# Kernel tuning notes

Measured on AMD Instinct MI355X. Metric: run time of the kernel, lower is better.

The kernel has to match this reference:

```python
import jax, jax.numpy as jnp
import numpy as np

T, H, E, F = 2048, 2048, 8, 4096  # tokens, hidden, experts, ffn per expert


def setup_inputs() -> dict:
    key = jax.random.key(0)
    ks = jax.random.split(key, 5)
    scale = 0.02
    return {
        "x": jax.random.normal(ks[0], (T, H), dtype=jnp.float32),
        "gate_w": jax.random.normal(ks[1], (E, H), dtype=jnp.float32) * scale,
        "w1": jax.random.normal(ks[2], (E * F, H), dtype=jnp.float32) * scale,
        "w2": jax.random.normal(ks[3], (E * F, H), dtype=jnp.float32) * scale,
        "w3": jax.random.normal(ks[4], (E * F, H), dtype=jnp.float32) * scale,
        "top_k": 2,
    }


def reference(x, gate_w, w1, w2, w3, top_k):
    # x: [T, H]; gate_w: [E, H]; w1/w2/w3: [E*F, H]
    t, h = x.shape
    e = gate_w.shape[0]
    f = w1.shape[0] // e

    # --- routing (matches select_experts / dense_forward gating) ---
    gate_logits = x @ gate_w.T                                   # [T, E]
    probs = jax.nn.softmax(gate_logits.astype(jnp.float32), axis=-1)
    vals, idx = jax.lax.top_k(probs, top_k)                      # [T, k]
    vals = vals / vals.sum(axis=-1, keepdims=True)               # renormalize
    w_full = jnp.zeros((t, e), dtype=probs.dtype)
    w_full = w_full.at[jnp.arange(t)[:, None], idx].set(vals)    # [T, E]

    # --- expert FFN: SwiGLU per expert (full-capacity, no token drop) ---
    w1r = w1.reshape(e, f, h)
    w3r = w3.reshape(e, f, h)
    w2r = w2.reshape(e, f, h)
    h1 = jnp.einsum('th,efh->etf', x, w1r)                       # [E, T, F]
    h3 = jnp.einsum('th,efh->etf', x, w3r)
    inter = jax.nn.silu(h1) * h3                                 # [E, T, F]
    out_e = jnp.einsum('etf,efh->eth', inter, w2r)               # [E, T, H]

    # --- combine with routing weights ---
    out = jnp.einsum('eth,te->th', out_e, w_full.astype(x.dtype))
    return out
```

## Files before the change

kernel.cpp:

```cpp
#include <hip/hip_runtime.h>
#include <cstdint>
#include <cstddef>

#define T_TOK 2048
#define H_DIM 2048
#define E_NUM 8
#define F_DIM 4096

typedef __attribute__((ext_vector_type(8))) short bh8;
typedef __attribute__((ext_vector_type(4))) float f32x4;

static __device__ __forceinline__ unsigned short f2bf(float f) {
  union { float f; unsigned int u; } v; v.f = f;
  unsigned int r = v.u + 0x7FFFu + ((v.u >> 16) & 1u);
  return (unsigned short)(r >> 16);
}

__global__ __launch_bounds__(256) void convert_x(const float* __restrict__ x,
                                                 unsigned short* __restrict__ xb) {
  size_t i = ((size_t)blockIdx.x * 256 + threadIdx.x) * 4;
  float4 v = *(const float4*)(x + i);
  ushort4 o;
  o.x = f2bf(v.x); o.y = f2bf(v.y); o.z = f2bf(v.z); o.w = f2bf(v.w);
  *(ushort4*)(xb + i) = o;
}

__global__ __launch_bounds__(64) void gate_topk(const float* __restrict__ x,
                                                const float* __restrict__ gw,
                                                int* __restrict__ counts,
                                                int* __restrict__ etok,
                                                float* __restrict__ ewts) {
  const int t = blockIdx.x;
  const int lane = threadIdx.x;
  float acc[E_NUM];
#pragma unroll
  for (int e = 0; e < E_NUM; e++) acc[e] = 0.f;
  const float* xr = x + (size_t)t * H_DIM;
  for (int i = lane; i < H_DIM; i += 64) {
    float xv = xr[i];
#pragma unroll
    for (int e = 0; e < E_NUM; e++) acc[e] += xv * gw[e * H_DIM + i];
  }
#pragma unroll
  for (int e = 0; e < E_NUM; e++) {
#pragma unroll
    for (int off = 32; off > 0; off >>= 1) acc[e] += __shfl_xor(acc[e], off, 64);
  }
  if (lane == 0) {
    int e0 = 0;
#pragma unroll
    for (int e = 1; e < E_NUM; e++) if (acc[e] > acc[e0]) e0 = e;
    int e1 = (e0 == 0) ? 1 : 0;
#pragma unroll
    for (int e = 0; e < E_NUM; e++) {
      if (e != e0 && acc[e] > acc[e1]) e1 = e;
    }
    float z = __expf(acc[e1] - acc[e0]);
    float w0 = 1.f / (1.f + z);
    float w1v = z / (1.f + z);
    int p0 = atomicAdd(&counts[e0], 1);
    etok[e0 * T_TOK + p0] = t; ewts[e0 * T_TOK + p0] = w0;
    int p1 = atomicAdd(&counts[e1], 1);
    etok[e1 * T_TOK + p1] = t; ewts[e1 * T_TOK + p1] = w1v;
  }
}

__global__ void scan_offsets(const int* __restrict__ counts, int* __restrict__ offsets) {
  if (threadIdx.x == 0 && blockIdx.x == 0) {
    int run = 0;
    for (int e = 0; e < E_NUM; e++) { offsets[e] = run; run += counts[e]; }
  }
}

__global__ __launch_bounds__(256) void gemm1_swiglu(
    const unsigned short* __restrict__ xb,
    const float* __restrict__ w1,
    const float* __restrict__ w3,
    const int* __restrict__ counts, const int* __restrict__ offsets,
    const int* __restrict__ etok,
    unsigned short* __restrict__ inter)
{
  const int e = blockIdx.z, mt = blockIdx.y, nt = blockIdx.x;
  const int cnt = counts[e];
  const int rem = cnt - mt * 128;
  if (rem <= 0) return;
  const int tid = threadIdx.x;
  const int lane = tid & 63;
  const int wv = tid >> 6;

  __shared__ alignas(16) unsigned short As[128][40];
  __shared__ alignas(16) unsigned short B1s[64][40];
  __shared__ alignas(16) unsigned short B3s[64][40];

  const int ar0 = tid >> 2;
  const int ar1 = 64 + (tid >> 2);
  const int ac8 = (tid & 3) * 8;
  const int tokbase = e * T_TOK + mt * 128;
  const int t0 = etok[tokbase + (ar0 < rem ? ar0 : rem - 1)];
  const int t1 = etok[tokbase + (ar1 < rem ? ar1 : rem - 1)];
  const unsigned short* a0p = xb + (size_t)t0 * H_DIM + ac8;
  const unsigned short* a1p = xb + (size_t)t1 * H_DIM + ac8;

  const int br0 = tid >> 3;
  const int br1 = 32 + (tid >> 3);
  const int bc4 = (tid & 7) * 4;
  const size_t wrow0 = ((size_t)(e * F_DIM + nt * 64 + br0)) * H_DIM + bc4;
  const size_t wrow1 = ((size_t)(e * F_DIM + nt * 64 + br1)) * H_DIM + bc4;

  const int wm = (wv >> 1) * 64;
  const int wn = (wv & 1) * 32;
  const int mrow = lane & 15;
  const int qk = (lane >> 4) * 8;

  f32x4 acc1[4][2], acc3[4][2];
#pragma unroll
  for (int i = 0; i < 4; i++)
#pragma unroll
    for (int j = 0; j < 2; j++) { acc1[i][j] = (f32x4)(0.f); acc3[i][j] = (f32x4)(0.f); }

  for (int k0 = 0; k0 < H_DIM; k0 += 32) {
    *(uint4*)&As[ar0][ac8] = *(const uint4*)(a0p + k0);
    *(uint4*)&As[ar1][ac8] = *(const uint4*)(a1p + k0);
    {
      float4 v0 = *(const float4*)(w1 + wrow0 + k0);
      float4 v1 = *(const float4*)(w1 + wrow1 + k0);
      float4 u0 = *(const float4*)(w3 + wrow0 + k0);
      float4 u1 = *(const float4*)(w3 + wrow1 + k0);
      ushort4 o;
      o.x = f2bf(v0.x); o.y = f2bf(v0.y); o.z = f2bf(v0.z); o.w = f2bf(v0.w);
      *(ushort4*)&B1s[br0][bc4] = o;
      o.x = f2bf(v1.x); o.y = f2bf(v1.y); o.z = f2bf(v1.z); o.w = f2bf(v1.w);
      *(ushort4*)&B1s[br1][bc4] = o;
      o.x = f2bf(u0.x); o.y = f2bf(u0.y); o.z = f2bf(u0.z); o.w = f2bf(u0.w);
      *(ushort4*)&B3s[br0][bc4] = o;
      o.x = f2bf(u1.x); o.y = f2bf(u1.y); o.z = f2bf(u1.z); o.w = f2bf(u1.w);
      *(ushort4*)&B3s[br1][bc4] = o;
    }
    __syncthreads();
    bh8 a[4], b1[2], b3[2];
#pragma unroll
    for (int i = 0; i < 4; i++) a[i] = *(const bh8*)&As[wm + i * 16 + mrow][qk];
#pragma unroll
    for (int j = 0; j < 2; j++) {
      b1[j] = *(const bh8*)&B1s[wn + j * 16 + mrow][qk];
      b3[j] = *(const bh8*)&B3s[wn + j * 16 + mrow][qk];
    }
#pragma unroll
    for (int i = 0; i < 4; i++)
#pragma unroll
      for (int j = 0; j < 2; j++) {
        acc1[i][j] = __builtin_amdgcn_mfma_f32_16x16x32_bf16(a[i], b1[j], acc1[i][j], 0, 0, 0);
        acc3[i][j] = __builtin_amdgcn_mfma_f32_16x16x32_bf16(a[i], b3[j], acc3[i][j], 0, 0, 0);
      }
    __syncthreads();
  }

  const int off = offsets[e];
  const int quad = lane >> 4;
#pragma unroll
  for (int i = 0; i < 4; i++) {
#pragma unroll
    for (int r = 0; r < 4; r++) {
      int m = wm + i * 16 + quad * 4 + r;
      if (m < rem) {
        size_t rowbase = (size_t)(off + mt * 128 + m) * F_DIM + nt * 64 + wn + mrow;
#pragma unroll
        for (int j = 0; j < 2; j++) {
          float c1 = acc1[i][j][r], c3 = acc3[i][j][r];
          float s = c1 / (1.f + __expf(-c1));
          inter[rowbase + j * 16] = f2bf(s * c3);
        }
      }
    }
  }
}

__global__ __launch_bounds__(256) void gemm2_scatter(
    const unsigned short* __restrict__ inter,
    const float* __restrict__ w2,
    const int* __restrict__ counts, const int* __restrict__ offsets,
    const int* __restrict__ etok, const float* __restrict__ ewts,
    float* __restrict__ out)
{
  const int e = blockIdx.z, mt = blockIdx.y, nt = blockIdx.x;
  const int cnt = counts[e];
  const int rem = cnt - mt * 128;
  if (rem <= 0) return;
  const int tid = threadIdx.x;
  const int lane = tid & 63;
  const int wv = tid >> 6;

  __shared__ alignas(16) unsigned short As[128][40];
  __shared__ alignas(16) unsigned short Bs[128][40];

  const int off = offsets[e];
  const int ar0 = tid >> 2;
  const int ar1 = 64 + (tid >> 2);
  const int ac8 = (tid & 3) * 8;
  const int g0 = off + mt * 128 + (ar0 < rem ? ar0 : rem - 1);
  const int g1 = off + mt * 128 + (ar1 < rem ? ar1 : rem - 1);
  const unsigned short* a0p = inter + (size_t)g0 * F_DIM + ac8;
  const unsigned short* a1p = inter + (size_t)g1 * F_DIM + ac8;

  const int bkr = tid >> 5;
  const int bc4 = (tid & 31) * 4;

  const int wm = (wv >> 1) * 64;
  const int wn = (wv & 1) * 64;
  const int mrow = lane & 15;
  const int qk = (lane >> 4) * 8;

  f32x4 acc[4][4];
#pragma unroll
  for (int i = 0; i < 4; i++)
#pragma unroll
    for (int j = 0; j < 4; j++) acc[i][j] = (f32x4)(0.f);

  for (int k0 = 0; k0 < F_DIM; k0 += 32) {
    *(uint4*)&As[ar0][ac8] = *(const uint4*)(a0p + k0);
    *(uint4*)&As[ar1][ac8] = *(const uint4*)(a1p + k0);
#pragma unroll
    for (int l = 0; l < 4; l++) {
      int krow = bkr + l * 8;
      float4 v = *(const float4*)(w2 + ((size_t)(e * F_DIM + k0 + krow)) * H_DIM + nt * 128 + bc4);
      Bs[bc4 + 0][krow] = f2bf(v.x);
      Bs[bc4 + 1][krow] = f2bf(v.y);
      Bs[bc4 + 2][krow] = f2bf(v.z);
      Bs[bc4 + 3][krow] = f2bf(v.w);
    }
    __syncthreads();
    bh8 a[4], b[4];
#pragma unroll
    for (int i = 0; i < 4; i++) a[i] = *(const bh8*)&As[wm + i * 16 + mrow][qk];
#pragma unroll
    for (int j = 0; j < 4; j++) b[j] = *(const bh8*)&Bs[wn + j * 16 + mrow][qk];
#pragma unroll
    for (int i = 0; i < 4; i++)
#pragma unroll
      for (int j = 0; j < 4; j++)
        acc[i][j] = __builtin_amdgcn_mfma_f32_16x16x32_bf16(a[i], b[j], acc[i][j], 0, 0, 0);
    __syncthreads();
  }

  const int quad = lane >> 4;
#pragma unroll
  for (int i = 0; i < 4; i++) {
#pragma unroll
    for (int r = 0; r < 4; r++) {
      int m = wm + i * 16 + quad * 4 + r;
      if (m < rem) {
        int slot = e * T_TOK + mt * 128 + m;
        int t = etok[slot];
        float wgt = ewts[slot];
        float* orow = out + (size_t)t * H_DIM + nt * 128 + wn + mrow;
#pragma unroll
        for (int j = 0; j < 4; j++) atomicAdd(orow + j * 16, wgt * acc[i][j][r]);
      }
    }
  }
}

extern "C" void kernel_launch(void* const* d_in, const int* in_sizes, int n_in,
                              void* d_out, int out_size, void* d_ws, size_t ws_size,
                              hipStream_t stream) {
  const float* x  = (const float*)d_in[0];
  const float* gw = (const float*)d_in[1];
  const float* w1 = (const float*)d_in[2];
  const float* w2 = (const float*)d_in[3];
  const float* w3 = (const float*)d_in[4];
  float* out = (float*)d_out;

  char* ws = (char*)d_ws;
  int* counts   = (int*)(ws + 0);
  int* offsets  = (int*)(ws + 64);
  int* etok     = (int*)(ws + 128);
  float* ewts   = (float*)(ws + 128 + 65536);
  unsigned short* xb    = (unsigned short*)(ws + 256 * 1024);
  unsigned short* inter = (unsigned short*)(ws + 256 * 1024 + 8 * 1024 * 1024);

  hipMemsetAsync(counts, 0, 64, stream);
  hipMemsetAsync(d_out, 0, (size_t)T_TOK * H_DIM * sizeof(float), stream);

  convert_x<<<(T_TOK * H_DIM) / (256 * 4), 256, 0, stream>>>(x, xb);
  gate_topk<<<T_TOK, 64, 0, stream>>>(x, gw, counts, etok, ewts);
  scan_offsets<<<1, 64, 0, stream>>>(counts, offsets);
  gemm1_swiglu<<<dim3(F_DIM / 64, 16, E_NUM), 256, 0, stream>>>(xb, w1, w3, counts, offsets, etok, inter);
  gemm2_scatter<<<dim3(H_DIM / 128, 16, E_NUM), 256, 0, stream>>>(inter, w2, counts, offsets, etok, ewts, out);
}
```

Before: 1.386 ms.

## Pre-convert expert weights to bf16 and pre-transpose w2 in workspace

Adds pre-pass kernels that convert w1 and w3 to bf16 and transpose plus convert w2 into a K-contiguous bf16 layout, when the workspace is large enough. The GEMM kernels then load bf16 tiles with 16-byte vector loads instead of converting fp32 per tile. Every expert weight tile is reread by up to 16 M-tile blocks, so converting once is meant to cut fp32 traffic and the strided scalar LDS writes in gemm2. The pre-pass still reads all 768MB of fp32 weights every call and writes bf16 copies, so it adds traffic of its own. The output atomics also switch to unsafeAtomicAdd for hardware float atomics.

```diff
diff --git a/kernel.cpp b/kernel.cpp
--- a/kernel.cpp
+++ b/kernel.cpp
@@ -16,13 +16,41 @@
   return (unsigned short)(r >> 16);
 }
 
-__global__ __launch_bounds__(256) void convert_x(const float* __restrict__ x,
-                                                 unsigned short* __restrict__ xb) {
+__global__ __launch_bounds__(256) void convert_f32_bf16(const float* __restrict__ src,
+                                                        unsigned short* __restrict__ dst) {
   size_t i = ((size_t)blockIdx.x * 256 + threadIdx.x) * 4;
-  float4 v = *(const float4*)(x + i);
+  float4 v = *(const float4*)(src + i);
   ushort4 o;
   o.x = f2bf(v.x); o.y = f2bf(v.y); o.z = f2bf(v.z); o.w = f2bf(v.w);
-  *(ushort4*)(xb + i) = o;
+  *(ushort4*)(dst + i) = o;
+}
+
+__global__ __launch_bounds__(256) void transpose_w2(const float* __restrict__ w2,
+                                                    unsigned short* __restrict__ w2t) {
+  const int e = blockIdx.z;
+  const int f0 = blockIdx.y * 64;
+  const int h0 = blockIdx.x * 64;
+  __shared__ float tile[64][65];
+  const int tid = threadIdx.x;
+  const int r = tid >> 4;
+  const int c4 = (tid & 15) * 4;
+#pragma unroll
+  for (int l = 0; l < 4; l++) {
+    int f = r + l * 16;
+    float4 v = *(const float4*)(w2 + ((size_t)(e * F_DIM + f0 + f)) * H_DIM + h0 + c4);
+    tile[f][c4 + 0] = v.x; tile[f][c4 + 1] = v.y; tile[f][c4 + 2] = v.z; tile[f][c4 + 3] = v.w;
+  }
+  __syncthreads();
+#pragma unroll
+  for (int l = 0; l < 4; l++) {
+    int h = r + l * 16;
+    ushort4 o;
+    o.x = f2bf(tile[c4 + 0][h]);
+    o.y = f2bf(tile[c4 + 1][h]);
+    o.z = f2bf(tile[c4 + 2][h]);
+    o.w = f2bf(tile[c4 + 3][h]);
+    *(ushort4*)(w2t + ((size_t)e * H_DIM + h0 + h) * F_DIM + f0 + c4) = o;
+  }
 }
 
 __global__ __launch_bounds__(64) void gate_topk(const float* __restrict__ x,
@@ -72,17 +100,17 @@
   }
 }
 
+template<bool BW>
 __global__ __launch_bounds__(256) void gemm1_swiglu(
     const unsigned short* __restrict__ xb,
-    const float* __restrict__ w1,
-    const float* __restrict__ w3,
+    const float* __restrict__ w1f, const float* __restrict__ w3f,
+    const unsigned short* __restrict__ w1b, const unsigned short* __restrict__ w3b,
     const int* __restrict__ counts, const int* __restrict__ offsets,
     const int* __restrict__ etok,
     unsigned short* __restrict__ inter)
 {
   const int e = blockIdx.z, mt = blockIdx.y, nt = blockIdx.x;
-  const int cnt = counts[e];
-  const int rem = cnt - mt * 128;
+  const int rem = counts[e] - mt * 128;
   if (rem <= 0) return;
   const int tid = threadIdx.x;
   const int lane = tid & 63;
@@ -92,8 +120,7 @@
   __shared__ alignas(16) unsigned short B1s[64][40];
   __shared__ alignas(16) unsigned short B3s[64][40];
 
-  const int ar0 = tid >> 2;
-  const int ar1 = 64 + (tid >> 2);
+  const int ar0 = tid >> 2, ar1 = 64 + (tid >> 2);
   const int ac8 = (tid & 3) * 8;
   const int tokbase = e * T_TOK + mt * 128;
   const int t0 = etok[tokbase + (ar0 < rem ? ar0 : rem - 1)];
@@ -101,12 +128,6 @@
   const unsigned short* a0p = xb + (size_t)t0 * H_DIM + ac8;
   const unsigned short* a1p = xb + (size_t)t1 * H_DIM + ac8;
 
-  const int br0 = tid >> 3;
-  const int br1 = 32 + (tid >> 3);
-  const int bc4 = (tid & 7) * 4;
-  const size_t wrow0 = ((size_t)(e * F_DIM + nt * 64 + br0)) * H_DIM + bc4;
-  const size_t wrow1 = ((size_t)(e * F_DIM + nt * 64 + br1)) * H_DIM + bc4;
-
   const int wm = (wv >> 1) * 64;
   const int wn = (wv & 1) * 32;
   const int mrow = lane & 15;
@@ -121,11 +142,21 @@
   for (int k0 = 0; k0 < H_DIM; k0 += 32) {
     *(uint4*)&As[ar0][ac8] = *(const uint4*)(a0p + k0);
     *(uint4*)&As[ar1][ac8] = *(const uint4*)(a1p + k0);
-    {
-      float4 v0 = *(const float4*)(w1 + wrow0 + k0);
-      float4 v1 = *(const float4*)(w1 + wrow1 + k0);
-      float4 u0 = *(const float4*)(w3 + wrow0 + k0);
-      float4 u1 = *(const float4*)(w3 + wrow1 + k0);
+    if constexpr (BW) {
+      const int br = tid >> 2;
+      const int bc8 = (tid & 3) * 8;
+      size_t wrow = ((size_t)(e * F_DIM + nt * 64 + br)) * H_DIM + bc8 + k0;
+      *(uint4*)&B1s[br][bc8] = *(const uint4*)(w1b + wrow);
+      *(uint4*)&B3s[br][bc8] = *(const uint4*)(w3b + wrow);
+    } else {
+      const int br0 = tid >> 3, br1 = 32 + (tid >> 3);
+      const int bc4 = (tid & 7) * 4;
+      size_t wrow0 = ((size_t)(e * F_DIM + nt * 64 + br0)) * H_DIM + bc4 + k0;
+      size_t wrow1 = ((size_t)(e * F_DIM + nt * 64 + br1)) * H_DIM + bc4 + k0;
+      float4 v0 = *(const float4*)(w1f + wrow0);
+      float4 v1 = *(const float4*)(w1f + wrow1);
+      float4 u0 = *(const float4*)(w3f + wrow0);
+      float4 u1 = *(const float4*)(w3f + wrow1);
       ushort4 o;
       o.x = f2bf(v0.x); o.y = f2bf(v0.y); o.z = f2bf(v0.z); o.w = f2bf(v0.w);
       *(ushort4*)&B1s[br0][bc4] = o;
@@ -175,16 +206,17 @@
   }
 }
 
+template<bool BW>
 __global__ __launch_bounds__(256) void gemm2_scatter(
     const unsigned short* __restrict__ inter,
-    const float* __restrict__ w2,
+    const float* __restrict__ w2f,
+    const unsigned short* __restrict__ w2t,
     const int* __restrict__ counts, const int* __restrict__ offsets,
     const int* __restrict__ etok, const float* __restrict__ ewts,
     float* __restrict__ out)
 {
   const int e = blockIdx.z, mt = blockIdx.y, nt = blockIdx.x;
-  const int cnt = counts[e];
-  const int rem = cnt - mt * 128;
+  const int rem = counts[e] - mt * 128;
   if (rem <= 0) return;
   const int tid = threadIdx.x;
   const int lane = tid & 63;
@@ -194,17 +226,13 @@
   __shared__ alignas(16) unsigned short Bs[128][40];
 
   const int off = offsets[e];
-  const int ar0 = tid >> 2;
-  const int ar1 = 64 + (tid >> 2);
+  const int ar0 = tid >> 2, ar1 = 64 + (tid >> 2);
   const int ac8 = (tid & 3) * 8;
   const int g0 = off + mt * 128 + (ar0 < rem ? ar0 : rem - 1);
   const int g1 = off + mt * 128 + (ar1 < rem ? ar1 : rem - 1);
   const unsigned short* a0p = inter + (size_t)g0 * F_DIM + ac8;
   const unsigned short* a1p = inter + (size_t)g1 * F_DIM + ac8;
 
-  const int bkr = tid >> 5;
-  const int bc4 = (tid & 31) * 4;
-
   const int wm = (wv >> 1) * 64;
   const int wn = (wv & 1) * 64;
   const int mrow = lane & 15;
@@ -219,14 +247,23 @@
   for (int k0 = 0; k0 < F_DIM; k0 += 32) {
     *(uint4*)&As[ar0][ac8] = *(const uint4*)(a0p + k0);
     *(uint4*)&As[ar1][ac8] = *(const uint4*)(a1p + k0);
-#pragma unroll
-    for (int l = 0; l < 4; l++) {
-      int krow = bkr + l * 8;
-      float4 v = *(const float4*)(w2 + ((size_t)(e * F_DIM + k0 + krow)) * H_DIM + nt * 128 + bc4);
-      Bs[bc4 + 0][krow] = f2bf(v.x);
-      Bs[bc4 + 1][krow] = f2bf(v.y);
-      Bs[bc4 + 2][krow] = f2bf(v.z);
-      Bs[bc4 + 3][krow] = f2bf(v.w);
+    if constexpr (BW) {
+      const unsigned short* bp0 = w2t + ((size_t)e * H_DIM + nt * 128 + ar0) * F_DIM + ac8;
+      const unsigned short* bp1 = w2t + ((size_t)e * H_DIM + nt * 128 + ar1) * F_DIM + ac8;
+      *(uint4*)&Bs[ar0][ac8] = *(const uint4*)(bp0 + k0);
+      *(uint4*)&Bs[ar1][ac8] = *(const uint4*)(bp1 + k0);
+    } else {
+      const int bkr = tid >> 5;
+      const int bc4 = (tid & 31) * 4;
+#pragma unroll
+      for (int l = 0; l < 4; l++) {
+        int krow = bkr + l * 8;
+        float4 v = *(const float4*)(w2f + ((size_t)(e * F_DIM + k0 + krow)) * H_DIM + nt * 128 + bc4);
+        Bs[bc4 + 0][krow] = f2bf(v.x);
+        Bs[bc4 + 1][krow] = f2bf(v.y);
+        Bs[bc4 + 2][krow] = f2bf(v.z);
+        Bs[bc4 + 3][krow] = f2bf(v.w);
+      }
     }
     __syncthreads();
     bh8 a[4], b[4];
@@ -254,7 +291,7 @@
         float wgt = ewts[slot];
         float* orow = out + (size_t)t * H_DIM + nt * 128 + wn + mrow;
 #pragma unroll
-        for (int j = 0; j < 4; j++) atomicAdd(orow + j * 16, wgt * acc[i][j][r]);
+        for (int j = 0; j < 4; j++) unsafeAtomicAdd(orow + j * 16, wgt * acc[i][j][r]);
       }
     }
   }
@@ -277,13 +314,44 @@
   float* ewts   = (float*)(ws + 128 + 65536);
   unsigned short* xb    = (unsigned short*)(ws + 256 * 1024);
   unsigned short* inter = (unsigned short*)(ws + 256 * 1024 + 8 * 1024 * 1024);
+  const size_t BASE_END = 256 * 1024 + 8ull * 1024 * 1024 + 33554432ull;
+  const size_t WB = (size_t)E_NUM * F_DIM * H_DIM * 2;
+  unsigned short* w2t = (unsigned short*)(ws + BASE_END);
+  unsigned short* w1b = (unsigned short*)(ws + BASE_END + WB);
+  unsigned short* w3b = (unsigned short*)(ws + BASE_END + 2 * WB);
+  const size_t MID  = BASE_END + WB;
+  const size_t FULL = BASE_END + 3 * WB;
+  const bool tA = ws_size >= MID;
+  const bool tB = ws_size >= FULL;
 
   hipMemsetAsync(counts, 0, 64, stream);
   hipMemsetAsync(d_out, 0, (size_t)T_TOK * H_DIM * sizeof(float), stream);
 
-  convert_x<<<(T_TOK * H_DIM) / (256 * 4), 256, 0, stream>>>(x, xb);
+  convert_f32_bf16<<<(T_TOK * H_DIM) / (256 * 4), 256, 0, stream>>>(x, xb);
   gate_topk<<<T_TOK, 64, 0, stream>>>(x, gw, counts, etok, ewts);
   scan_offsets<<<1, 64, 0, stream>>>(counts, offsets);
-  gemm1_swiglu<<<dim3(F_DIM / 64, 16, E_NUM), 256, 0, stream>>>(xb, w1, w3, counts, offsets, etok, inter);
-  gemm2_scatter<<<dim3(H_DIM / 128, 16, E_NUM), 256, 0, stream>>>(inter, w2, counts, offsets, etok, ewts, out);
-}
+
+  const int WBLK = (E_NUM * F_DIM * H_DIM) / (256 * 4);
+  if (tB) {
+    convert_f32_bf16<<<WBLK, 256, 0, stream>>>(w1, w1b);
+    convert_f32_bf16<<<WBLK, 256, 0, stream>>>(w3, w3b);
+  }
+  if (tA) {
+    transpose_w2<<<dim3(H_DIM / 64, F_DIM / 64, E_NUM), 256, 0, stream>>>(w2, w2t);
+  }
+
+  if (tB) {
+    gemm1_swiglu<true><<<dim3(F_DIM / 64, 16, E_NUM), 256, 0, stream>>>(
+        xb, w1, w3, w1b, w3b, counts, offsets, etok, inter);
+  } else {
+    gemm1_swiglu<false><<<dim3(F_DIM / 64, 16, E_NUM), 256, 0, stream>>>(
+        xb, w1, w3, w1b, w3b, counts, offsets, etok, inter);
+  }
+  if (tA) {
+    gemm2_scatter<true><<<dim3(H_DIM / 128, 16, E_NUM), 256, 0, stream>>>(
+        inter, w2, w2t, counts, offsets, etok, ewts, out);
+  } else {
+    gemm2_scatter<false><<<dim3(H_DIM / 128, 16, E_NUM), 256, 0, stream>>>(
+        inter, w2, w2t, counts, offsets, etok, ewts, out);
+  }
+}
```

New measurement: 1.192 ms. -14.0%, faster.
